# Kernel optimization log

Measured on AMD Instinct MI355X. Metric: run time of the kernel, lower is better.

The kernel has to match this reference:

```python
import jax, jax.numpy as jnp
import numpy as np

FILL = -1000.0


def setup_inputs() -> dict:
    key = jax.random.key(0)
    k1, k2, k3 = jax.random.split(key, 3)
    B, T, L = 512, 512, 126
    emissions = jax.random.normal(k1, (B, T, L), dtype=jnp.float32)
    labels = jax.random.randint(k2, (B, T), 0, L, dtype=jnp.int32)
    transitions = jax.random.normal(k3, (L + 2, L + 2), dtype=jnp.float32)
    # mask: nothing transitions INTO start; nothing transitions OUT of end
    transitions = transitions.at[:, L].set(FILL).at[L + 1, :].set(FILL)
    return {"emissions": emissions, "labels": labels, "transitions": transitions}


def _expand_emission(emission, L):
    # emission: [T, L] -> [T+2, L+2] with START/END pseudo-observations
    T = emission.shape[0]
    pad = jnp.full((T, 2), FILL, dtype=emission.dtype)
    e = jnp.concatenate([emission, pad], axis=1)
    b_s = jnp.full((1, L + 2), FILL, dtype=emission.dtype).at[0, L].set(0.0)
    e_s = jnp.full((1, L + 2), FILL, dtype=emission.dtype).at[0, L + 1].set(0.0)
    return jnp.concatenate([b_s, e, e_s], axis=0)


def _total_path_score(emission, transitions, L):
    # Faithful to the original _log_sum_exp: per-column max, but the log term
    # sums exp over the WHOLE matrix (scalar), added to every column max.
    E = _expand_emission(emission, L)  # [T+2, L+2]

    def step(pre, obs):
        score = obs[None, :] + pre[:, None] + transitions  # [L+2, L+2]
        m = jnp.max(score, axis=0)                         # [L+2]
        pre_new = m + jnp.log(jnp.sum(jnp.exp(score - m[None, :])))
        return pre_new, None

    pre, _ = jax.lax.scan(step, E[0], E[1:])
    m = jnp.max(pre)
    return m + jnp.log(jnp.sum(jnp.exp(pre - m)))


def _real_path_score(emission, labels, transitions, L):
    T = emission.shape[0]
    em = jnp.sum(emission[jnp.arange(T), labels])
    seq = jnp.concatenate([
        jnp.array([L], dtype=labels.dtype), labels,
        jnp.array([L + 1], dtype=labels.dtype)
    ])
    tr = jnp.sum(transitions[seq[:-1], seq[1:]])
    return em + tr


def reference(emissions, labels, transitions):
    L = emissions.shape[-1]
    total = jax.vmap(lambda e: _total_path_score(e, transitions, L))(emissions)
    real = jax.vmap(lambda e, y: _real_path_score(e, y, transitions, L))(emissions, labels)
    return jnp.sum(total - real)
```

## Files before the change

kernel.cpp:

```cpp
#include <hip/hip_runtime.h>
#include <hip/hip_fp16.h>

#define NB 512
#define NT 512
#define NL 126
#define NS 128
#define SIGMA 0.0625f

typedef _Float16 h2 __attribute__((ext_vector_type(2)));

static __device__ __forceinline__ int pk_from(float a, float b) {
  return __builtin_bit_cast(int, __builtin_amdgcn_cvt_pkrtz(a, b));
}
static __device__ __forceinline__ int pkmul(int a, int b) {
  int d; asm("v_pk_mul_f16 %0, %1, %2" : "=v"(d) : "v"(a), "v"(b)); return d;
}
static __device__ __forceinline__ int pkmax(int a, int b) {
  int d; asm("v_pk_max_f16 %0, %1, %2" : "=v"(d) : "v"(a), "v"(b)); return d;
}
static __device__ __forceinline__ int pkadd(int a, int b) {
  int d; asm("v_pk_add_f16 %0, %1, %2" : "=v"(d) : "v"(a), "v"(b)); return d;
}
static __device__ __forceinline__ int dppswap(int x) {
  return __builtin_amdgcn_update_dpp(0, x, 0xB1, 0xf, 0xf, false);
}

#define DPP_ADD(x, ctrl, rm) \
  ((x) + __int_as_float(__builtin_amdgcn_update_dpp(0, __float_as_int(x), (ctrl), (rm), 0xf, false)))
#define WAVE_ADD(x) do { \
  x = DPP_ADD(x, 0x111, 0xf); x = DPP_ADD(x, 0x112, 0xf); \
  x = DPP_ADD(x, 0x114, 0xf); x = DPP_ADD(x, 0x118, 0xf); \
  x = DPP_ADD(x, 0x142, 0xa); x = DPP_ADD(x, 0x143, 0xc); } while (0)

__global__ __launch_bounds__(256) void crf_kernel(
    const float* __restrict__ emissions,
    const int*   __restrict__ labels,
    const float* __restrict__ trans,
    float*       __restrict__ out)
{
  const int b   = blockIdx.x;
  const int tid = threadIdx.x;
  const int wv  = tid >> 6;
  const int ln  = tid & 63;
  const int col = (wv << 5) | (ln >> 1);
  const int rh  = ln & 1;

  __shared__ __align__(16) _Float16 u_sh[2 * NS];
  __shared__ __align__(16) float sPart[2][4];
  __shared__ __align__(16) float zPart[2][4];
  __shared__ float fin[4];

  const float* em  = emissions + (size_t)b * NT * NL;
  const int*   lab = labels + b * NT;

  float tau = -3.0e38f;
  for (int i = 0; i < NS; i++) tau = fmaxf(tau, trans[i * NS + col]);

  int tab[32];
  #pragma unroll
  for (int k = 0; k < 32; k++) {
    int row = rh * 64 + 2 * k;
    float t0 = __expf(trans[row * NS + col] - tau);
    float t1 = __expf(trans[(row + 1) * NS + col] - tau);
    tab[k] = pk_from(t0, t1);
  }

  float realp = 0.f;
  #pragma unroll
  for (int q = 0; q < NT / 256; q++) {
    int t  = tid + q * 256;
    int lt = lab[t];
    int nx = (t + 1 < NT) ? lab[t + 1] : (NL + 1);
    realp += em[t * NL + lt] + trans[lt * NS + nx];
  }
  if (tid == 0) realp += trans[NL * NS + lab[0]];

  if (tid < NS) {
    u_sh[tid]      = (_Float16)((tid == NL) ? 1.f : 0.f);
    u_sh[NS + tid] = (_Float16)0.f;
  }
  float Q = 0.f, Cc = 0.f;
  float emc = (col < NL) ? em[col] : 0.f;
  float emn = (col < NL) ? em[NL + col] : 0.f;
  __syncthreads();

  for (int t = 0; t <= NT; t++) {
    float r;
    if (t > 0) {
      const float4 sp = *(const float4*)sPart[t & 1];
      const float4 zp = *(const float4*)zPart[t & 1];
      float S = 0.5f * ((sp.x + sp.y) + (sp.z + sp.w));
      float Z = 0.5f * ((zp.x + zp.y) + (zp.z + zp.w));
      Cc += __logf(S);
      Q  += __logf(Z);
      r = SIGMA * __builtin_amdgcn_rcpf(Z);
    } else {
      r = SIGMA;
    }

    float obsv;
    if (t < NT) obsv = (col < NL) ? emc : -1000.f;
    else        obsv = (col == NL + 1) ? 0.f : -1000.f;
    float g = __expf(obsv + tau);
    float emf = (t + 2 < NT && col < NL) ? em[(t + 2) * NL + col] : 0.f;
    emc = emn; emn = emf;

    const int4* up = (const int4*)(u_sh + (t & 1) * NS) + rh * 8;
    int hA = 0, hB = 0, hC = 0, hD = 0;
    int sA = 0, sB = 0, sC = 0, sD = 0;
    #pragma unroll
    for (int kk = 0; kk < 8; kk++) {
      int4 uu = up[kk];
      int m0 = pkmul(uu.x, tab[4 * kk + 0]);
      int m1 = pkmul(uu.y, tab[4 * kk + 1]);
      int m2 = pkmul(uu.z, tab[4 * kk + 2]);
      int m3 = pkmul(uu.w, tab[4 * kk + 3]);
      hA = pkmax(hA, m0); hB = pkmax(hB, m1);
      hC = pkmax(hC, m2); hD = pkmax(hD, m3);
      sA = pkadd(sA, m0); sB = pkadd(sB, m1);
      sC = pkadd(sC, m2); sD = pkadd(sD, m3);
    }
    int hv = pkmax(pkmax(hA, hB), pkmax(hC, hD));
    int sv = pkadd(pkadd(sA, sB), pkadd(sC, sD));
    hv = pkmax(hv, dppswap(hv));
    sv = pkadd(sv, dppswap(sv));
    h2 hh = __builtin_bit_cast(h2, hv);
    h2 ss = __builtin_bit_cast(h2, sv);
    float h = fmaxf(fmaxf((float)hh.x, (float)hh.y), 1e-30f);
    float s = (float)ss.x + (float)ss.y;

    float w = h * g;
    float v = w * r;
    u_sh[((t + 1) & 1) * NS + col] = (_Float16)v;

    float contrib = s * __builtin_amdgcn_rcpf(h);
    float cS = contrib, cV = v;
    WAVE_ADD(cS);
    WAVE_ADD(cV);
    if (ln == 63) {
      sPart[(t + 1) & 1][wv] = cS;
      zPart[(t + 1) & 1][wv] = cV;
    }
    __syncthreads();
  }

  {
    const float4 sp = *(const float4*)sPart[1];
    const float4 zp = *(const float4*)zPart[1];
    float S = 0.5f * ((sp.x + sp.y) + (sp.z + sp.w));
    float Z = 0.5f * ((zp.x + zp.y) + (zp.z + zp.w));
    Cc += __logf(S);
    Q  += __logf(Z);
  }

  WAVE_ADD(realp);
  if (ln == 63) fin[wv] = realp;
  __syncthreads();
  if (tid == 0) {
    const float CONST = 513.f * 2.772588722f;
    float total = Cc + Q + CONST;
    atomicAdd(out, total - ((fin[0] + fin[1]) + (fin[2] + fin[3])));
  }
}

extern "C" void kernel_launch(void* const* d_in, const int* in_sizes, int n_in,
                              void* d_out, int out_size, void* d_ws, size_t ws_size,
                              hipStream_t stream) {
  const float* em  = (const float*)d_in[0];
  const int*   lab = (const int*)d_in[1];
  const float* tr  = (const float*)d_in[2];
  (void)hipMemsetAsync(d_out, 0, sizeof(float), stream);
  crf_kernel<<<NB, 256, 0, stream>>>(em, lab, tr, (float*)d_out);
}
```

Measured before the change: 635.9 us.

## Process two sequences per block to interleave independent recurrences

Each block now runs the forward recurrence for two batch elements at once. Both share the transition table held in registers and a single barrier per time step, which roughly halves the number of serialized barrier/latency chains per element and gives the scheduler independent work to fill pipeline stalls. The DPP reductions and swaps are also rewritten as inline asm with fused v_add_f32_dpp. The cost is a grid of only 256 blocks on a 256-CU device, so per-CU occupancy drops, plus higher register pressure from the 16 int4 LDS loads per step.

```diff
diff --git a/kernel.cpp b/kernel.cpp
--- a/kernel.cpp
+++ b/kernel.cpp
@@ -22,15 +22,20 @@
   int d; asm("v_pk_add_f16 %0, %1, %2" : "=v"(d) : "v"(a), "v"(b)); return d;
 }
 static __device__ __forceinline__ int dppswap(int x) {
-  return __builtin_amdgcn_update_dpp(0, x, 0xB1, 0xf, 0xf, false);
-}
-
-#define DPP_ADD(x, ctrl, rm) \
-  ((x) + __int_as_float(__builtin_amdgcn_update_dpp(0, __float_as_int(x), (ctrl), (rm), 0xf, false)))
+  int d;
+  asm("v_mov_b32_dpp %0, %1 quad_perm:[1,0,3,2] row_mask:0xf bank_mask:0xf"
+      : "=v"(d) : "v"(x));
+  return d;
+}
+
 #define WAVE_ADD(x) do { \
-  x = DPP_ADD(x, 0x111, 0xf); x = DPP_ADD(x, 0x112, 0xf); \
-  x = DPP_ADD(x, 0x114, 0xf); x = DPP_ADD(x, 0x118, 0xf); \
-  x = DPP_ADD(x, 0x142, 0xa); x = DPP_ADD(x, 0x143, 0xc); } while (0)
+  asm("v_add_f32_dpp %0, %0, %0 row_shr:1  row_mask:0xf bank_mask:0xf bound_ctrl:0" : "+v"(x)); \
+  asm("v_add_f32_dpp %0, %0, %0 row_shr:2  row_mask:0xf bank_mask:0xf bound_ctrl:0" : "+v"(x)); \
+  asm("v_add_f32_dpp %0, %0, %0 row_shr:4  row_mask:0xf bank_mask:0xf bound_ctrl:0" : "+v"(x)); \
+  asm("v_add_f32_dpp %0, %0, %0 row_shr:8  row_mask:0xf bank_mask:0xf bound_ctrl:0" : "+v"(x)); \
+  asm("v_add_f32_dpp %0, %0, %0 row_bcast:15 row_mask:0xa bank_mask:0xf bound_ctrl:0" : "+v"(x)); \
+  asm("v_add_f32_dpp %0, %0, %0 row_bcast:31 row_mask:0xc bank_mask:0xf bound_ctrl:0" : "+v"(x)); \
+} while (0)
 
 __global__ __launch_bounds__(256) void crf_kernel(
     const float* __restrict__ emissions,
@@ -38,20 +43,24 @@
     const float* __restrict__ trans,
     float*       __restrict__ out)
 {
-  const int b   = blockIdx.x;
+  const int bid = blockIdx.x;
+  const int b0  = 2 * bid;
+  const int b1  = 2 * bid + 1;
   const int tid = threadIdx.x;
   const int wv  = tid >> 6;
   const int ln  = tid & 63;
   const int col = (wv << 5) | (ln >> 1);
   const int rh  = ln & 1;
 
-  __shared__ __align__(16) _Float16 u_sh[2 * NS];
-  __shared__ __align__(16) float sPart[2][4];
-  __shared__ __align__(16) float zPart[2][4];
-  __shared__ float fin[4];
-
-  const float* em  = emissions + (size_t)b * NT * NL;
-  const int*   lab = labels + b * NT;
+  __shared__ __align__(16) _Float16 u_sh[2][2 * NS];
+  __shared__ __align__(16) float sPart[2][2][4];
+  __shared__ __align__(16) float zPart[2][2][4];
+  __shared__ float fin[2][4];
+
+  const float* emA  = emissions + (size_t)b0 * NT * NL;
+  const float* emB  = emissions + (size_t)b1 * NT * NL;
+  const int*   labA = labels + b0 * NT;
+  const int*   labB = labels + b1 * NT;
 
   float tau = -3.0e38f;
   for (int i = 0; i < NS; i++) tau = fmaxf(tau, trans[i * NS + col]);
@@ -65,101 +74,172 @@
     tab[k] = pk_from(t0, t1);
   }
 
-  float realp = 0.f;
+  float realpA = 0.f, realpB = 0.f;
   #pragma unroll
   for (int q = 0; q < NT / 256; q++) {
     int t  = tid + q * 256;
-    int lt = lab[t];
-    int nx = (t + 1 < NT) ? lab[t + 1] : (NL + 1);
-    realp += em[t * NL + lt] + trans[lt * NS + nx];
-  }
-  if (tid == 0) realp += trans[NL * NS + lab[0]];
+    int la = labA[t];
+    int na = (t + 1 < NT) ? labA[t + 1] : (NL + 1);
+    realpA += emA[t * NL + la] + trans[la * NS + na];
+    int lb = labB[t];
+    int nb = (t + 1 < NT) ? labB[t + 1] : (NL + 1);
+    realpB += emB[t * NL + lb] + trans[lb * NS + nb];
+  }
+  if (tid == 0) {
+    realpA += trans[NL * NS + labA[0]];
+    realpB += trans[NL * NS + labB[0]];
+  }
 
   if (tid < NS) {
-    u_sh[tid]      = (_Float16)((tid == NL) ? 1.f : 0.f);
-    u_sh[NS + tid] = (_Float16)0.f;
-  }
-  float Q = 0.f, Cc = 0.f;
-  float emc = (col < NL) ? em[col] : 0.f;
-  float emn = (col < NL) ? em[NL + col] : 0.f;
+    _Float16 d = (_Float16)((tid == NL) ? 1.f : 0.f);
+    u_sh[0][tid] = d; u_sh[0][NS + tid] = (_Float16)0.f;
+    u_sh[1][tid] = d; u_sh[1][NS + tid] = (_Float16)0.f;
+  }
+  float QA = 0.f, CcA = 0.f, QB = 0.f, CcB = 0.f;
+  float emcA = (col < NL) ? emA[col] : 0.f;
+  float emnA = (col < NL) ? emA[NL + col] : 0.f;
+  float emcB = (col < NL) ? emB[col] : 0.f;
+  float emnB = (col < NL) ? emB[NL + col] : 0.f;
   __syncthreads();
 
   for (int t = 0; t <= NT; t++) {
-    float r;
+    const int sl = t & 1;
+
+    float rA, rB;
     if (t > 0) {
-      const float4 sp = *(const float4*)sPart[t & 1];
-      const float4 zp = *(const float4*)zPart[t & 1];
-      float S = 0.5f * ((sp.x + sp.y) + (sp.z + sp.w));
-      float Z = 0.5f * ((zp.x + zp.y) + (zp.z + zp.w));
-      Cc += __logf(S);
-      Q  += __logf(Z);
-      r = SIGMA * __builtin_amdgcn_rcpf(Z);
+      const float4 spA = *(const float4*)sPart[0][sl];
+      const float4 zpA = *(const float4*)zPart[0][sl];
+      const float4 spB = *(const float4*)sPart[1][sl];
+      const float4 zpB = *(const float4*)zPart[1][sl];
+      float SA = 0.5f * ((spA.x + spA.y) + (spA.z + spA.w));
+      float ZA = 0.5f * ((zpA.x + zpA.y) + (zpA.z + zpA.w));
+      float SB = 0.5f * ((spB.x + spB.y) + (spB.z + spB.w));
+      float ZB = 0.5f * ((zpB.x + zpB.y) + (zpB.z + zpB.w));
+      CcA += __logf(SA);
+      QA  += __logf(ZA);
+      CcB += __logf(SB);
+      QB  += __logf(ZB);
+      rA = SIGMA * __builtin_amdgcn_rcpf(ZA);
+      rB = SIGMA * __builtin_amdgcn_rcpf(ZB);
     } else {
-      r = SIGMA;
-    }
-
-    float obsv;
-    if (t < NT) obsv = (col < NL) ? emc : -1000.f;
-    else        obsv = (col == NL + 1) ? 0.f : -1000.f;
-    float g = __expf(obsv + tau);
-    float emf = (t + 2 < NT && col < NL) ? em[(t + 2) * NL + col] : 0.f;
-    emc = emn; emn = emf;
-
-    const int4* up = (const int4*)(u_sh + (t & 1) * NS) + rh * 8;
-    int hA = 0, hB = 0, hC = 0, hD = 0;
-    int sA = 0, sB = 0, sC = 0, sD = 0;
+      rA = SIGMA; rB = SIGMA;
+    }
+
+    float obsA, obsB;
+    if (t < NT) {
+      obsA = (col < NL) ? emcA : -1000.f;
+      obsB = (col < NL) ? emcB : -1000.f;
+    } else {
+      obsA = (col == NL + 1) ? 0.f : -1000.f;
+      obsB = obsA;
+    }
+    float gA = __expf(obsA + tau);
+    float gB = __expf(obsB + tau);
+    float efA = (t + 2 < NT && col < NL) ? emA[(t + 2) * NL + col] : 0.f;
+    float efB = (t + 2 < NT && col < NL) ? emB[(t + 2) * NL + col] : 0.f;
+    emcA = emnA; emnA = efA;
+    emcB = emnB; emnB = efB;
+
+    const int4* upA = (const int4*)(&u_sh[0][sl * NS]) + rh * 8;
+    const int4* upB = (const int4*)(&u_sh[1][sl * NS]) + rh * 8;
+    int4 ua[8], ub[8];
+    #pragma unroll
+    for (int k = 0; k < 8; k++) ua[k] = upA[k];
+    #pragma unroll
+    for (int k = 0; k < 8; k++) ub[k] = upB[k];
+
+    int hA0 = 0, hB0 = 0, hC0 = 0, hD0 = 0;
+    int sA0 = 0, sB0 = 0, sC0 = 0, sD0 = 0;
     #pragma unroll
     for (int kk = 0; kk < 8; kk++) {
-      int4 uu = up[kk];
-      int m0 = pkmul(uu.x, tab[4 * kk + 0]);
-      int m1 = pkmul(uu.y, tab[4 * kk + 1]);
-      int m2 = pkmul(uu.z, tab[4 * kk + 2]);
-      int m3 = pkmul(uu.w, tab[4 * kk + 3]);
-      hA = pkmax(hA, m0); hB = pkmax(hB, m1);
-      hC = pkmax(hC, m2); hD = pkmax(hD, m3);
-      sA = pkadd(sA, m0); sB = pkadd(sB, m1);
-      sC = pkadd(sC, m2); sD = pkadd(sD, m3);
-    }
-    int hv = pkmax(pkmax(hA, hB), pkmax(hC, hD));
-    int sv = pkadd(pkadd(sA, sB), pkadd(sC, sD));
-    hv = pkmax(hv, dppswap(hv));
-    sv = pkadd(sv, dppswap(sv));
-    h2 hh = __builtin_bit_cast(h2, hv);
-    h2 ss = __builtin_bit_cast(h2, sv);
-    float h = fmaxf(fmaxf((float)hh.x, (float)hh.y), 1e-30f);
-    float s = (float)ss.x + (float)ss.y;
-
-    float w = h * g;
-    float v = w * r;
-    u_sh[((t + 1) & 1) * NS + col] = (_Float16)v;
-
-    float contrib = s * __builtin_amdgcn_rcpf(h);
-    float cS = contrib, cV = v;
-    WAVE_ADD(cS);
-    WAVE_ADD(cV);
+      int m0 = pkmul(ua[kk].x, tab[4 * kk + 0]);
+      int m1 = pkmul(ua[kk].y, tab[4 * kk + 1]);
+      int m2 = pkmul(ua[kk].z, tab[4 * kk + 2]);
+      int m3 = pkmul(ua[kk].w, tab[4 * kk + 3]);
+      hA0 = pkmax(hA0, m0); hB0 = pkmax(hB0, m1);
+      hC0 = pkmax(hC0, m2); hD0 = pkmax(hD0, m3);
+      sA0 = pkadd(sA0, m0); sB0 = pkadd(sB0, m1);
+      sC0 = pkadd(sC0, m2); sD0 = pkadd(sD0, m3);
+    }
+    int hvA = pkmax(pkmax(hA0, hB0), pkmax(hC0, hD0));
+    int svA = pkadd(pkadd(sA0, sB0), pkadd(sC0, sD0));
+    hvA = pkmax(hvA, dppswap(hvA));
+    svA = pkadd(svA, dppswap(svA));
+    h2 hhA = __builtin_bit_cast(h2, hvA);
+    h2 ssA = __builtin_bit_cast(h2, svA);
+    float hAf = fmaxf(fmaxf((float)hhA.x, (float)hhA.y), 1e-30f);
+    float sAf = (float)ssA.x + (float)ssA.y;
+    float wA = hAf * gA;
+    float vA = wA * rA;
+    u_sh[0][((t + 1) & 1) * NS + col] = (_Float16)vA;
+    float cSA = sAf * __builtin_amdgcn_rcpf(hAf);
+    float cVA = vA;
+
+    int hA1 = 0, hB1 = 0, hC1 = 0, hD1 = 0;
+    int sA1 = 0, sB1 = 0, sC1 = 0, sD1 = 0;
+    #pragma unroll
+    for (int kk = 0; kk < 8; kk++) {
+      int m0 = pkmul(ub[kk].x, tab[4 * kk + 0]);
+      int m1 = pkmul(ub[kk].y, tab[4 * kk + 1]);
+      int m2 = pkmul(ub[kk].z, tab[4 * kk + 2]);
+      int m3 = pkmul(ub[kk].w, tab[4 * kk + 3]);
+      hA1 = pkmax(hA1, m0); hB1 = pkmax(hB1, m1);
+      hC1 = pkmax(hC1, m2); hD1 = pkmax(hD1, m3);
+      sA1 = pkadd(sA1, m0); sB1 = pkadd(sB1, m1);
+      sC1 = pkadd(sC1, m2); sD1 = pkadd(sD1, m3);
+    }
+    int hvB = pkmax(pkmax(hA1, hB1), pkmax(hC1, hD1));
+    int svB = pkadd(pkadd(sA1, sB1), pkadd(sC1, sD1));
+    hvB = pkmax(hvB, dppswap(hvB));
+    svB = pkadd(svB, dppswap(svB));
+    h2 hhB = __builtin_bit_cast(h2, hvB);
+    h2 ssB = __builtin_bit_cast(h2, svB);
+    float hBf = fmaxf(fmaxf((float)hhB.x, (float)hhB.y), 1e-30f);
+    float sBf = (float)ssB.x + (float)ssB.y;
+    float wB = hBf * gB;
+    float vB = wB * rB;
+    u_sh[1][((t + 1) & 1) * NS + col] = (_Float16)vB;
+    float cSB = sBf * __builtin_amdgcn_rcpf(hBf);
+    float cVB = vB;
+
+    WAVE_ADD(cSA);
+    WAVE_ADD(cVA);
+    WAVE_ADD(cSB);
+    WAVE_ADD(cVB);
     if (ln == 63) {
-      sPart[(t + 1) & 1][wv] = cS;
-      zPart[(t + 1) & 1][wv] = cV;
+      const int s2 = (t + 1) & 1;
+      sPart[0][s2][wv] = cSA; zPart[0][s2][wv] = cVA;
+      sPart[1][s2][wv] = cSB; zPart[1][s2][wv] = cVB;
     }
     __syncthreads();
   }
 
   {
-    const float4 sp = *(const float4*)sPart[1];
-    const float4 zp = *(const float4*)zPart[1];
-    float S = 0.5f * ((sp.x + sp.y) + (sp.z + sp.w));
-    float Z = 0.5f * ((zp.x + zp.y) + (zp.z + zp.w));
-    Cc += __logf(S);
-    Q  += __logf(Z);
-  }
-
-  WAVE_ADD(realp);
-  if (ln == 63) fin[wv] = realp;
+    const float4 spA = *(const float4*)sPart[0][1];
+    const float4 zpA = *(const float4*)zPart[0][1];
+    const float4 spB = *(const float4*)sPart[1][1];
+    const float4 zpB = *(const float4*)zPart[1][1];
+    float SA = 0.5f * ((spA.x + spA.y) + (spA.z + spA.w));
+    float ZA = 0.5f * ((zpA.x + zpA.y) + (zpA.z + zpA.w));
+    float SB = 0.5f * ((spB.x + spB.y) + (spB.z + spB.w));
+    float ZB = 0.5f * ((zpB.x + zpB.y) + (zpB.z + zpB.w));
+    CcA += __logf(SA);
+    QA  += __logf(ZA);
+    CcB += __logf(SB);
+    QB  += __logf(ZB);
+  }
+
+  WAVE_ADD(realpA);
+  WAVE_ADD(realpB);
+  if (ln == 63) { fin[0][wv] = realpA; fin[1][wv] = realpB; }
   __syncthreads();
   if (tid == 0) {
     const float CONST = 513.f * 2.772588722f;
-    float total = Cc + Q + CONST;
-    atomicAdd(out, total - ((fin[0] + fin[1]) + (fin[2] + fin[3])));
+    float totA  = CcA + QA + CONST;
+    float totB  = CcB + QB + CONST;
+    float realA = (fin[0][0] + fin[0][1]) + (fin[0][2] + fin[0][3]);
+    float realB = (fin[1][0] + fin[1][1]) + (fin[1][2] + fin[1][3]);
+    atomicAdd(out, (totA - realA) + (totB - realB));
   }
 }
 
@@ -170,5 +250,5 @@
   const int*   lab = (const int*)d_in[1];
   const float* tr  = (const float*)d_in[2];
   (void)hipMemsetAsync(d_out, 0, sizeof(float), stream);
-  crf_kernel<<<NB, 256, 0, stream>>>(em, lab, tr, (float*)d_out);
-}
+  crf_kernel<<<NB / 2, 256, 0, stream>>>(em, lab, tr, (float*)d_out);
+}
```

After: 726.3 us. 1.14x slower.

## Run each batch CRF recurrence in a single wave without block barriers

Applied to the files above, without the earlier changes.

Each sequence's forward recurrence moves from a 256-thread block to one 64-lane wave. Each lane owns two columns and the full 128-row transition table, held as two 64-entry packed-half register arrays. This drops the per-timestep __syncthreads and the cross-wave partial-sum exchange through shared memory; wave reductions and shuffles are used instead. It quadruples per-lane arithmetic and register pressure, and leaves 512 single-wave blocks, so occupancy and latency hiding may suffer. The LDS write-then-read of u inside a single wave now relies on implicit wave ordering with no barrier.

```diff
diff --git a/kernel.cpp b/kernel.cpp
--- a/kernel.cpp
+++ b/kernel.cpp
@@ -12,6 +12,10 @@
 static __device__ __forceinline__ int pk_from(float a, float b) {
   return __builtin_bit_cast(int, __builtin_amdgcn_cvt_pkrtz(a, b));
 }
+static __device__ __forceinline__ int pk_rne(float a, float b) {
+  h2 p; p.x = (_Float16)a; p.y = (_Float16)b;
+  return __builtin_bit_cast(int, p);
+}
 static __device__ __forceinline__ int pkmul(int a, int b) {
   int d; asm("v_pk_mul_f16 %0, %1, %2" : "=v"(d) : "v"(a), "v"(b)); return d;
 }
@@ -21,145 +25,149 @@
 static __device__ __forceinline__ int pkadd(int a, int b) {
   int d; asm("v_pk_add_f16 %0, %1, %2" : "=v"(d) : "v"(a), "v"(b)); return d;
 }
-static __device__ __forceinline__ int dppswap(int x) {
-  return __builtin_amdgcn_update_dpp(0, x, 0xB1, 0xf, 0xf, false);
-}
 
-#define DPP_ADD(x, ctrl, rm) \
-  ((x) + __int_as_float(__builtin_amdgcn_update_dpp(0, __float_as_int(x), (ctrl), (rm), 0xf, false)))
 #define WAVE_ADD(x) do { \
-  x = DPP_ADD(x, 0x111, 0xf); x = DPP_ADD(x, 0x112, 0xf); \
-  x = DPP_ADD(x, 0x114, 0xf); x = DPP_ADD(x, 0x118, 0xf); \
-  x = DPP_ADD(x, 0x142, 0xa); x = DPP_ADD(x, 0x143, 0xc); } while (0)
+  asm("v_add_f32_dpp %0, %0, %0 row_shr:1  row_mask:0xf bank_mask:0xf bound_ctrl:0" : "+v"(x)); \
+  asm("v_add_f32_dpp %0, %0, %0 row_shr:2  row_mask:0xf bank_mask:0xf bound_ctrl:0" : "+v"(x)); \
+  asm("v_add_f32_dpp %0, %0, %0 row_shr:4  row_mask:0xf bank_mask:0xf bound_ctrl:0" : "+v"(x)); \
+  asm("v_add_f32_dpp %0, %0, %0 row_shr:8  row_mask:0xf bank_mask:0xf bound_ctrl:0" : "+v"(x)); \
+  asm("v_add_f32_dpp %0, %0, %0 row_bcast:15 row_mask:0xa bank_mask:0xf bound_ctrl:0" : "+v"(x)); \
+  asm("v_add_f32_dpp %0, %0, %0 row_bcast:31 row_mask:0xc bank_mask:0xf bound_ctrl:0" : "+v"(x)); \
+} while (0)
 
-__global__ __launch_bounds__(256) void crf_kernel(
+__global__ __launch_bounds__(64, 1) void crf_kernel(
     const float* __restrict__ emissions,
     const int*   __restrict__ labels,
     const float* __restrict__ trans,
     float*       __restrict__ out)
 {
   const int b   = blockIdx.x;
-  const int tid = threadIdx.x;
-  const int wv  = tid >> 6;
-  const int ln  = tid & 63;
-  const int col = (wv << 5) | (ln >> 1);
-  const int rh  = ln & 1;
+  const int ln  = threadIdx.x;
+  const int c0  = 2 * ln;
+  const int c1  = c0 + 1;
+  const bool has = (ln < 63);
 
-  __shared__ __align__(16) _Float16 u_sh[2 * NS];
-  __shared__ __align__(16) float sPart[2][4];
-  __shared__ __align__(16) float zPart[2][4];
-  __shared__ float fin[4];
+  __shared__ __align__(16) int u_lds[64];
 
   const float* em  = emissions + (size_t)b * NT * NL;
-  const int*   lab = labels + b * NT;
+  const int*   lab = labels + (size_t)b * NT;
 
-  float tau = -3.0e38f;
-  for (int i = 0; i < NS; i++) tau = fmaxf(tau, trans[i * NS + col]);
+  float tau0 = -3.0e38f, tau1 = -3.0e38f;
+  for (int rr = 0; rr < NS; rr++) {
+    float2 tr = *(const float2*)&trans[rr * NS + c0];
+    tau0 = fmaxf(tau0, tr.x);
+    tau1 = fmaxf(tau1, tr.y);
+  }
 
-  int tab[32];
+  int tabA[64], tabB[64];
   #pragma unroll
-  for (int k = 0; k < 32; k++) {
-    int row = rh * 64 + 2 * k;
-    float t0 = __expf(trans[row * NS + col] - tau);
-    float t1 = __expf(trans[(row + 1) * NS + col] - tau);
-    tab[k] = pk_from(t0, t1);
+  for (int k = 0; k < 64; k++) {
+    float2 r0 = *(const float2*)&trans[(2 * k) * NS + c0];
+    float2 r1 = *(const float2*)&trans[(2 * k + 1) * NS + c0];
+    tabA[k] = pk_from(__expf(r0.x - tau0), __expf(r1.x - tau0));
+    tabB[k] = pk_from(__expf(r0.y - tau1), __expf(r1.y - tau1));
   }
 
   float realp = 0.f;
   #pragma unroll
-  for (int q = 0; q < NT / 256; q++) {
-    int t  = tid + q * 256;
-    int lt = lab[t];
-    int nx = (t + 1 < NT) ? lab[t + 1] : (NL + 1);
-    realp += em[t * NL + lt] + trans[lt * NS + nx];
+  for (int q = 0; q < 8; q++) {
+    int t  = ln + q * 64;
+    int la = lab[t];
+    int na = (t + 1 < NT) ? lab[t + 1] : (NL + 1);
+    realp += em[t * NL + la] + trans[la * NS + na];
   }
-  if (tid == 0) realp += trans[NL * NS + lab[0]];
+  if (ln == 0) realp += trans[NL * NS + lab[0]];
 
-  if (tid < NS) {
-    u_sh[tid]      = (_Float16)((tid == NL) ? 1.f : 0.f);
-    u_sh[NS + tid] = (_Float16)0.f;
+  u_lds[ln] = (ln == 63) ? pk_rne(1.f, 0.f) : 0;
+
+  float2 emc, emn;
+  if (has) {
+    emc = *(const float2*)&em[c0];
+    emn = *(const float2*)&em[NL + c0];
+  } else {
+    emc.x = emc.y = 0.f; emn.x = emn.y = 0.f;
   }
-  float Q = 0.f, Cc = 0.f;
-  float emc = (col < NL) ? em[col] : 0.f;
-  float emn = (col < NL) ? em[NL + col] : 0.f;
-  __syncthreads();
 
+  int4 uu[16];
+  {
+    const int4* up = (const int4*)u_lds;
+    #pragma unroll
+    for (int j = 0; j < 16; j++) uu[j] = up[j];
+  }
+
+  float Cc = 0.f, Q = 0.f, r = SIGMA;
+
+  #pragma unroll 1
   for (int t = 0; t <= NT; t++) {
-    float r;
-    if (t > 0) {
-      const float4 sp = *(const float4*)sPart[t & 1];
-      const float4 zp = *(const float4*)zPart[t & 1];
-      float S = 0.5f * ((sp.x + sp.y) + (sp.z + sp.w));
-      float Z = 0.5f * ((zp.x + zp.y) + (zp.z + zp.w));
-      Cc += __logf(S);
-      Q  += __logf(Z);
-      r = SIGMA * __builtin_amdgcn_rcpf(Z);
+    float obs0, obs1;
+    if (t < NT) {
+      obs0 = has ? emc.x : -1000.f;
+      obs1 = has ? emc.y : -1000.f;
     } else {
-      r = SIGMA;
+      obs0 = -1000.f;
+      obs1 = (ln == 63) ? 0.f : -1000.f;
+    }
+    float g0 = __expf(obs0 + tau0);
+    float g1 = __expf(obs1 + tau1);
+
+    float2 ef;
+    if (t + 2 < NT && has) ef = *(const float2*)&em[(t + 2) * NL + c0];
+    else { ef.x = 0.f; ef.y = 0.f; }
+    emc = emn; emn = ef;
+
+    int h0a=0,h0b=0,h0c=0,h0d=0, s0a=0,s0b=0,s0c=0,s0d=0;
+    int h1a=0,h1b=0,h1c=0,h1d=0, s1a=0,s1b=0,s1c=0,s1d=0;
+    #pragma unroll
+    for (int j = 0; j < 16; j++) {
+      int m;
+      m = pkmul(uu[j].x, tabA[4*j+0]); h0a = pkmax(h0a,m); s0a = pkadd(s0a,m);
+      m = pkmul(uu[j].y, tabA[4*j+1]); h0b = pkmax(h0b,m); s0b = pkadd(s0b,m);
+      m = pkmul(uu[j].z, tabA[4*j+2]); h0c = pkmax(h0c,m); s0c = pkadd(s0c,m);
+      m = pkmul(uu[j].w, tabA[4*j+3]); h0d = pkmax(h0d,m); s0d = pkadd(s0d,m);
+      m = pkmul(uu[j].x, tabB[4*j+0]); h1a = pkmax(h1a,m); s1a = pkadd(s1a,m);
+      m = pkmul(uu[j].y, tabB[4*j+1]); h1b = pkmax(h1b,m); s1b = pkadd(s1b,m);
+      m = pkmul(uu[j].z, tabB[4*j+2]); h1c = pkmax(h1c,m); s1c = pkadd(s1c,m);
+      m = pkmul(uu[j].w, tabB[4*j+3]); h1d = pkmax(h1d,m); s1d = pkadd(s1d,m);
+    }
+    int hv0 = pkmax(pkmax(h0a,h0b), pkmax(h0c,h0d));
+    int sv0 = pkadd(pkadd(s0a,s0b), pkadd(s0c,s0d));
+    int hv1 = pkmax(pkmax(h1a,h1b), pkmax(h1c,h1d));
+    int sv1 = pkadd(pkadd(s1a,s1b), pkadd(s1c,s1d));
+    h2 hh0 = __builtin_bit_cast(h2, hv0);
+    h2 ss0 = __builtin_bit_cast(h2, sv0);
+    h2 hh1 = __builtin_bit_cast(h2, hv1);
+    h2 ss1 = __builtin_bit_cast(h2, sv1);
+    float h0 = fmaxf(fmaxf((float)hh0.x, (float)hh0.y), 1e-30f);
+    float s0 = (float)ss0.x + (float)ss0.y;
+    float h1 = fmaxf(fmaxf((float)hh1.x, (float)hh1.y), 1e-30f);
+    float s1 = (float)ss1.x + (float)ss1.y;
+
+    float w0 = h0 * g0, v0 = w0 * r;
+    float w1 = h1 * g1, v1 = w1 * r;
+
+    u_lds[ln] = pk_rne(v0, v1);
+    {
+      const int4* up = (const int4*)u_lds;
+      #pragma unroll
+      for (int j = 0; j < 16; j++) uu[j] = up[j];
     }
 
-    float obsv;
-    if (t < NT) obsv = (col < NL) ? emc : -1000.f;
-    else        obsv = (col == NL + 1) ? 0.f : -1000.f;
-    float g = __expf(obsv + tau);
-    float emf = (t + 2 < NT && col < NL) ? em[(t + 2) * NL + col] : 0.f;
-    emc = emn; emn = emf;
-
-    const int4* up = (const int4*)(u_sh + (t & 1) * NS) + rh * 8;
-    int hA = 0, hB = 0, hC = 0, hD = 0;
-    int sA = 0, sB = 0, sC = 0, sD = 0;
-    #pragma unroll
-    for (int kk = 0; kk < 8; kk++) {
-      int4 uu = up[kk];
-      int m0 = pkmul(uu.x, tab[4 * kk + 0]);
-      int m1 = pkmul(uu.y, tab[4 * kk + 1]);
-      int m2 = pkmul(uu.z, tab[4 * kk + 2]);
-      int m3 = pkmul(uu.w, tab[4 * kk + 3]);
-      hA = pkmax(hA, m0); hB = pkmax(hB, m1);
-      hC = pkmax(hC, m2); hD = pkmax(hD, m3);
-      sA = pkadd(sA, m0); sB = pkadd(sB, m1);
-      sC = pkadd(sC, m2); sD = pkadd(sD, m3);
-    }
-    int hv = pkmax(pkmax(hA, hB), pkmax(hC, hD));
-    int sv = pkadd(pkadd(sA, sB), pkadd(sC, sD));
-    hv = pkmax(hv, dppswap(hv));
-    sv = pkadd(sv, dppswap(sv));
-    h2 hh = __builtin_bit_cast(h2, hv);
-    h2 ss = __builtin_bit_cast(h2, sv);
-    float h = fmaxf(fmaxf((float)hh.x, (float)hh.y), 1e-30f);
-    float s = (float)ss.x + (float)ss.y;
-
-    float w = h * g;
-    float v = w * r;
-    u_sh[((t + 1) & 1) * NS + col] = (_Float16)v;
-
-    float contrib = s * __builtin_amdgcn_rcpf(h);
-    float cS = contrib, cV = v;
-    WAVE_ADD(cS);
-    WAVE_ADD(cV);
-    if (ln == 63) {
-      sPart[(t + 1) & 1][wv] = cS;
-      zPart[(t + 1) & 1][wv] = cV;
-    }
-    __syncthreads();
-  }
-
-  {
-    const float4 sp = *(const float4*)sPart[1];
-    const float4 zp = *(const float4*)zPart[1];
-    float S = 0.5f * ((sp.x + sp.y) + (sp.z + sp.w));
-    float Z = 0.5f * ((zp.x + zp.y) + (zp.z + zp.w));
+    float contrib = s0 * __builtin_amdgcn_rcpf(h0)
+                  + s1 * __builtin_amdgcn_rcpf(h1);
+    float zz = v0 + v1;
+    WAVE_ADD(contrib);
+    WAVE_ADD(zz);
+    float S = __shfl(contrib, 63);
+    float Z = __shfl(zz, 63);
     Cc += __logf(S);
     Q  += __logf(Z);
+    r = SIGMA * __builtin_amdgcn_rcpf(Z);
   }
 
   WAVE_ADD(realp);
-  if (ln == 63) fin[wv] = realp;
-  __syncthreads();
-  if (tid == 0) {
+  if (ln == 63) {
     const float CONST = 513.f * 2.772588722f;
-    float total = Cc + Q + CONST;
-    atomicAdd(out, total - ((fin[0] + fin[1]) + (fin[2] + fin[3])));
+    atomicAdd(out, (Cc + Q + CONST) - realp);
   }
 }
 
@@ -170,5 +178,5 @@
   const int*   lab = (const int*)d_in[1];
   const float* tr  = (const float*)d_in[2];
   (void)hipMemsetAsync(d_out, 0, sizeof(float), stream);
-  crf_kernel<<<NB, 256, 0, stream>>>(em, lab, tr, (float*)d_out);
+  crf_kernel<<<NB, 64, 0, stream>>>(em, lab, tr, (float*)d_out);
 }
```

Result: slower. 743.1 us (+16.9%).

## Use one thread per column with 128-thread blocks and inline-asm DPP reductions

Applied to the files above, without the earlier changes.

Each block now runs 128 threads, each owning a full column, instead of 256 threads that split each column into two row halves. That removes the cross-lane DPP swap merge and halves the partial sums reduced per step. Each thread now holds a 64-entry packed transition table and does twice the packed-FP16 work per step, which serialises more of the recurrence per lane. The wave reductions are rewritten as inline v_add_f32_dpp asm, the block is pinned to one wave per EU, and the time loop is unrolled by two.

```diff
diff --git a/kernel.cpp b/kernel.cpp
--- a/kernel.cpp
+++ b/kernel.cpp
@@ -21,18 +21,18 @@
 static __device__ __forceinline__ int pkadd(int a, int b) {
   int d; asm("v_pk_add_f16 %0, %1, %2" : "=v"(d) : "v"(a), "v"(b)); return d;
 }
-static __device__ __forceinline__ int dppswap(int x) {
-  return __builtin_amdgcn_update_dpp(0, x, 0xB1, 0xf, 0xf, false);
-}
 
-#define DPP_ADD(x, ctrl, rm) \
-  ((x) + __int_as_float(__builtin_amdgcn_update_dpp(0, __float_as_int(x), (ctrl), (rm), 0xf, false)))
 #define WAVE_ADD(x) do { \
-  x = DPP_ADD(x, 0x111, 0xf); x = DPP_ADD(x, 0x112, 0xf); \
-  x = DPP_ADD(x, 0x114, 0xf); x = DPP_ADD(x, 0x118, 0xf); \
-  x = DPP_ADD(x, 0x142, 0xa); x = DPP_ADD(x, 0x143, 0xc); } while (0)
+  asm("v_add_f32_dpp %0, %0, %0 row_shr:1  row_mask:0xf bank_mask:0xf bound_ctrl:0" : "+v"(x)); \
+  asm("v_add_f32_dpp %0, %0, %0 row_shr:2  row_mask:0xf bank_mask:0xf bound_ctrl:0" : "+v"(x)); \
+  asm("v_add_f32_dpp %0, %0, %0 row_shr:4  row_mask:0xf bank_mask:0xf bound_ctrl:0" : "+v"(x)); \
+  asm("v_add_f32_dpp %0, %0, %0 row_shr:8  row_mask:0xf bank_mask:0xf bound_ctrl:0" : "+v"(x)); \
+  asm("v_add_f32_dpp %0, %0, %0 row_bcast:15 row_mask:0xa bank_mask:0xf bound_ctrl:0" : "+v"(x)); \
+  asm("v_add_f32_dpp %0, %0, %0 row_bcast:31 row_mask:0xc bank_mask:0xf bound_ctrl:0" : "+v"(x)); \
+} while (0)
 
-__global__ __launch_bounds__(256) void crf_kernel(
+__global__ __launch_bounds__(128) __attribute__((amdgpu_waves_per_eu(1, 1)))
+void crf_kernel(
     const float* __restrict__ emissions,
     const int*   __restrict__ labels,
     const float* __restrict__ trans,
@@ -42,55 +42,54 @@
   const int tid = threadIdx.x;
   const int wv  = tid >> 6;
   const int ln  = tid & 63;
-  const int col = (wv << 5) | (ln >> 1);
-  const int rh  = ln & 1;
+  const int col = tid;
+  const bool has = (col < NL);
 
-  __shared__ __align__(16) _Float16 u_sh[2 * NS];
-  __shared__ __align__(16) float sPart[2][4];
-  __shared__ __align__(16) float zPart[2][4];
-  __shared__ float fin[4];
+  __shared__ __align__(16) _Float16 u_sh[2][NS];
+  __shared__ float sPart[2][2];
+  __shared__ float zPart[2][2];
+  __shared__ float fin[2];
 
   const float* em  = emissions + (size_t)b * NT * NL;
-  const int*   lab = labels + b * NT;
+  const int*   lab = labels + (size_t)b * NT;
 
   float tau = -3.0e38f;
-  for (int i = 0; i < NS; i++) tau = fmaxf(tau, trans[i * NS + col]);
+  for (int rr = 0; rr < NS; rr++) tau = fmaxf(tau, trans[rr * NS + col]);
 
-  int tab[32];
+  int tab[64];
   #pragma unroll
-  for (int k = 0; k < 32; k++) {
-    int row = rh * 64 + 2 * k;
-    float t0 = __expf(trans[row * NS + col] - tau);
-    float t1 = __expf(trans[(row + 1) * NS + col] - tau);
+  for (int k = 0; k < 64; k++) {
+    float t0 = __expf(trans[(2 * k) * NS + col] - tau);
+    float t1 = __expf(trans[(2 * k + 1) * NS + col] - tau);
     tab[k] = pk_from(t0, t1);
   }
 
   float realp = 0.f;
   #pragma unroll
-  for (int q = 0; q < NT / 256; q++) {
-    int t  = tid + q * 256;
-    int lt = lab[t];
-    int nx = (t + 1 < NT) ? lab[t + 1] : (NL + 1);
-    realp += em[t * NL + lt] + trans[lt * NS + nx];
+  for (int q = 0; q < NT / 128; q++) {
+    int t  = tid + q * 128;
+    int la = lab[t];
+    int na = (t + 1 < NT) ? lab[t + 1] : (NL + 1);
+    realp += em[t * NL + la] + trans[la * NS + na];
   }
   if (tid == 0) realp += trans[NL * NS + lab[0]];
 
-  if (tid < NS) {
-    u_sh[tid]      = (_Float16)((tid == NL) ? 1.f : 0.f);
-    u_sh[NS + tid] = (_Float16)0.f;
-  }
-  float Q = 0.f, Cc = 0.f;
-  float emc = (col < NL) ? em[col] : 0.f;
-  float emn = (col < NL) ? em[NL + col] : 0.f;
+  u_sh[0][col] = (_Float16)((col == NL) ? 1.f : 0.f);
+
+  float emc = has ? em[col] : 0.f;
+  float emn = has ? em[NL + col] : 0.f;
+
+  float Cc = 0.f, Q = 0.f;
   __syncthreads();
 
+  #pragma unroll 2
   for (int t = 0; t <= NT; t++) {
+    const int sl = t & 1;
+
     float r;
     if (t > 0) {
-      const float4 sp = *(const float4*)sPart[t & 1];
-      const float4 zp = *(const float4*)zPart[t & 1];
-      float S = 0.5f * ((sp.x + sp.y) + (sp.z + sp.w));
-      float Z = 0.5f * ((zp.x + zp.y) + (zp.z + zp.w));
+      float S = sPart[sl][0] + sPart[sl][1];
+      float Z = zPart[sl][0] + zPart[sl][1];
       Cc += __logf(S);
       Q  += __logf(Z);
       r = SIGMA * __builtin_amdgcn_rcpf(Z);
@@ -98,32 +97,31 @@
       r = SIGMA;
     }
 
-    float obsv;
-    if (t < NT) obsv = (col < NL) ? emc : -1000.f;
-    else        obsv = (col == NL + 1) ? 0.f : -1000.f;
-    float g = __expf(obsv + tau);
-    float emf = (t + 2 < NT && col < NL) ? em[(t + 2) * NL + col] : 0.f;
-    emc = emn; emn = emf;
+    float obs;
+    if (t < NT) obs = has ? emc : -1000.f;
+    else        obs = (col == NL + 1) ? 0.f : -1000.f;
+    float g = __expf(obs + tau);
 
-    const int4* up = (const int4*)(u_sh + (t & 1) * NS) + rh * 8;
-    int hA = 0, hB = 0, hC = 0, hD = 0;
-    int sA = 0, sB = 0, sC = 0, sD = 0;
+    float ef = (t + 2 < NT && has) ? em[(t + 2) * NL + col] : 0.f;
+    emc = emn; emn = ef;
+
+    const int4* up = (const int4*)u_sh[sl];
+    int4 uu[16];
     #pragma unroll
-    for (int kk = 0; kk < 8; kk++) {
-      int4 uu = up[kk];
-      int m0 = pkmul(uu.x, tab[4 * kk + 0]);
-      int m1 = pkmul(uu.y, tab[4 * kk + 1]);
-      int m2 = pkmul(uu.z, tab[4 * kk + 2]);
-      int m3 = pkmul(uu.w, tab[4 * kk + 3]);
-      hA = pkmax(hA, m0); hB = pkmax(hB, m1);
-      hC = pkmax(hC, m2); hD = pkmax(hD, m3);
-      sA = pkadd(sA, m0); sB = pkadd(sB, m1);
-      sC = pkadd(sC, m2); sD = pkadd(sD, m3);
+    for (int j = 0; j < 16; j++) uu[j] = up[j];
+
+    int ha = 0, hb = 0, hcc = 0, hd = 0;
+    int sa = 0, sb = 0, scc = 0, sd = 0;
+    #pragma unroll
+    for (int j = 0; j < 16; j++) {
+      int m;
+      m = pkmul(uu[j].x, tab[4*j+0]); ha  = pkmax(ha,  m); sa  = pkadd(sa,  m);
+      m = pkmul(uu[j].y, tab[4*j+1]); hb  = pkmax(hb,  m); sb  = pkadd(sb,  m);
+      m = pkmul(uu[j].z, tab[4*j+2]); hcc = pkmax(hcc, m); scc = pkadd(scc, m);
+      m = pkmul(uu[j].w, tab[4*j+3]); hd  = pkmax(hd,  m); sd  = pkadd(sd,  m);
     }
-    int hv = pkmax(pkmax(hA, hB), pkmax(hC, hD));
-    int sv = pkadd(pkadd(sA, sB), pkadd(sC, sD));
-    hv = pkmax(hv, dppswap(hv));
-    sv = pkadd(sv, dppswap(sv));
+    int hv = pkmax(pkmax(ha, hb), pkmax(hcc, hd));
+    int sv = pkadd(pkadd(sa, sb), pkadd(scc, sd));
     h2 hh = __builtin_bit_cast(h2, hv);
     h2 ss = __builtin_bit_cast(h2, sv);
     float h = fmaxf(fmaxf((float)hh.x, (float)hh.y), 1e-30f);
@@ -131,24 +129,22 @@
 
     float w = h * g;
     float v = w * r;
-    u_sh[((t + 1) & 1) * NS + col] = (_Float16)v;
+    u_sh[sl ^ 1][col] = (_Float16)v;
 
     float contrib = s * __builtin_amdgcn_rcpf(h);
-    float cS = contrib, cV = v;
-    WAVE_ADD(cS);
-    WAVE_ADD(cV);
+    float zz = v;
+    WAVE_ADD(contrib);
+    WAVE_ADD(zz);
     if (ln == 63) {
-      sPart[(t + 1) & 1][wv] = cS;
-      zPart[(t + 1) & 1][wv] = cV;
+      sPart[sl ^ 1][wv] = contrib;
+      zPart[sl ^ 1][wv] = zz;
     }
     __syncthreads();
   }
 
   {
-    const float4 sp = *(const float4*)sPart[1];
-    const float4 zp = *(const float4*)zPart[1];
-    float S = 0.5f * ((sp.x + sp.y) + (sp.z + sp.w));
-    float Z = 0.5f * ((zp.x + zp.y) + (zp.z + zp.w));
+    float S = sPart[1][0] + sPart[1][1];
+    float Z = zPart[1][0] + zPart[1][1];
     Cc += __logf(S);
     Q  += __logf(Z);
   }
@@ -158,8 +154,7 @@
   __syncthreads();
   if (tid == 0) {
     const float CONST = 513.f * 2.772588722f;
-    float total = Cc + Q + CONST;
-    atomicAdd(out, total - ((fin[0] + fin[1]) + (fin[2] + fin[3])));
+    atomicAdd(out, (Cc + Q + CONST) - (fin[0] + fin[1]));
   }
 }
 
@@ -170,5 +165,5 @@
   const int*   lab = (const int*)d_in[1];
   const float* tr  = (const float*)d_in[2];
   (void)hipMemsetAsync(d_out, 0, sizeof(float), stream);
-  crf_kernel<<<NB, 256, 0, stream>>>(em, lab, tr, (float*)d_out);
+  crf_kernel<<<NB, 128, 0, stream>>>(em, lab, tr, (float*)d_out);
 }
```

Result: faster. 577.5 us (-9.2%).
